# Kernel optimization log

Measured on AMD Instinct MI355X. Metric: run time of the kernel, lower is better.

The kernel has to match this reference:

```python
import jax, jax.numpy as jnp
import numpy as np

N = 50000      # nodes
E = 800000     # edges (avg degree 16)
D_IN = 64      # input feature dim
HID = 128      # hidden dim
NEG = 0.2      # LeakyReLU slope (PyG GATConv default)
EPS = 1e-5     # BatchNorm eps


def _bn(x, g, b):
    mu = jnp.mean(x, 0)
    var = jnp.var(x, 0)
    return (x - mu) * jax.lax.rsqrt(var + EPS) * g + b


def _gat(x, src, dst, W, a_s, a_d, bias, heads, out_c, concat):
    # PyG GATConv: h = xW per head, e_ij = LeakyReLU(a_s.h_i + a_d.h_j),
    # softmax over incoming edges of each dst node, weighted scatter-sum.
    n = x.shape[0]
    h = (x @ W).reshape(n, heads, out_c)                 # [N,H,C]
    sc_s = jnp.sum(h * a_s, -1)                          # [N,H]
    sc_d = jnp.sum(h * a_d, -1)                          # [N,H]
    e = jax.nn.leaky_relu(sc_s[src] + sc_d[dst], NEG)    # [E,H]
    m = jax.lax.stop_gradient(jax.ops.segment_max(e, dst, num_segments=n))
    e = jnp.exp(e - m[dst])
    s = jax.ops.segment_sum(e, dst, num_segments=n)
    alpha = e / (s[dst] + 1e-16)                         # [E,H]
    out = jax.ops.segment_sum(h[src] * alpha[:, :, None], dst, num_segments=n)
    out = out.reshape(n, heads * out_c) if concat else out.mean(1)
    return out + bias


def setup_inputs() -> dict:
    ks = jax.random.split(jax.random.key(0), 20)
    r = lambda i, sh, s=0.05: jax.random.normal(ks[i], sh, jnp.float32) * s
    return dict(
        x=jax.random.normal(ks[0], (N, D_IN), jnp.float32),
        edge_index=jax.random.randint(ks[1], (2, E), 0, N, dtype=jnp.int32),
        in_gamma=jnp.ones((D_IN,)), in_beta=jnp.zeros((D_IN,)),
        proj_W=r(2, (D_IN, HID)), proj_b=jnp.zeros((HID,)),
        skip_W=r(3, (HID, HID)), skip_b=jnp.zeros((HID,)),
        conv1_W=r(4, (HID, HID)), conv1_as=r(5, (4, 32)), conv1_ad=r(6, (4, 32)), conv1_b=jnp.zeros((HID,)),
        bn1_g=jnp.ones((HID,)), bn1_b=jnp.zeros((HID,)),
        conv2_W=r(7, (HID, HID)), conv2_as=r(8, (4, 32)), conv2_ad=r(9, (4, 32)), conv2_b=jnp.zeros((HID,)),
        bn2_g=jnp.ones((HID,)), bn2_b=jnp.zeros((HID,)),
        conv3_W=r(10, (HID, HID)), conv3_as=r(11, (1, HID)), conv3_ad=r(12, (1, HID)), conv3_b=jnp.zeros((HID,)),
        bn3_g=jnp.ones((HID,)), bn3_b=jnp.zeros((HID,)),
        cls_W1=r(13, (HID, 64)), cls_b1=jnp.zeros((64,)),
        cls_W2=r(14, (64, 32)), cls_b2=jnp.zeros((32,)),
        cls_W3=r(15, (32, 2)), cls_b3=jnp.zeros((2,)),
        conf_W=r(16, (HID, 1)), conf_b=jnp.zeros((1,)),
    )


def reference(x, edge_index, in_gamma, in_beta, proj_W, proj_b, skip_W, skip_b,
              conv1_W, conv1_as, conv1_ad, conv1_b, bn1_g, bn1_b,
              conv2_W, conv2_as, conv2_ad, conv2_b, bn2_g, bn2_b,
              conv3_W, conv3_as, conv3_ad, conv3_b, bn3_g, bn3_b,
              cls_W1, cls_b1, cls_W2, cls_b2, cls_W3, cls_b3, conf_W, conf_b):
    n = x.shape[0]
    # PyG GATConv add_self_loops=True
    loop = jnp.arange(n, dtype=edge_index.dtype)
    src = jnp.concatenate([edge_index[0], loop])
    dst = jnp.concatenate([edge_index[1], loop])

    h = _bn(x, in_gamma, in_beta)
    h = h @ proj_W + proj_b
    hr = jax.nn.relu(h)
    h_skip = hr @ skip_W + skip_b

    h = _gat(hr, src, dst, conv1_W, conv1_as, conv1_ad, conv1_b, 4, 32, True)
    h = jax.nn.relu(_bn(h, bn1_g, bn1_b))
    h = _gat(h, src, dst, conv2_W, conv2_as, conv2_ad, conv2_b, 4, 32, True)
    h = jax.nn.relu(_bn(h, bn2_g, bn2_b))
    h = _gat(h, src, dst, conv3_W, conv3_as, conv3_ad, conv3_b, 1, HID, False)
    h = jax.nn.relu(_bn(h, bn3_g, bn3_b) + h_skip)

    c = jax.nn.relu(h @ cls_W1 + cls_b1)
    c = jax.nn.relu(c @ cls_W2 + cls_b2)
    logits = c @ cls_W3 + cls_b3
    conf = jax.nn.sigmoid(h @ conf_W + conf_b)
    return logits, conf
```

## Files before the change

### kernel.cpp

```cpp
#include <hip/hip_runtime.h>
#include <cstdint>
#include <cstddef>

#define NN 50000
#define EE 800000
#define TOT_E (NN + EE)
#define NBK 391
#define BCAP 2560

typedef __attribute__((ext_vector_type(8))) short short8;
typedef __attribute__((ext_vector_type(4))) float f32x4;

static __device__ __forceinline__ unsigned short f2bf(float f) {
  union { float f; unsigned u; } v;
  v.f = f;
  unsigned r = v.u + 0x7FFFu + ((v.u >> 16) & 1u);
  return (unsigned short)(r >> 16);
}
static __device__ __forceinline__ float bf2f(unsigned short u) {
  union { unsigned u; float f; } v;
  v.u = ((unsigned)u) << 16;
  return v.f;
}
static __device__ __forceinline__ float bf2f_lo(unsigned u) {
  union { unsigned u; float f; } v;
  v.u = u << 16;
  return v.f;
}
static __device__ __forceinline__ float bf2f_hi(unsigned u) {
  union { unsigned u; float f; } v;
  v.u = u & 0xFFFF0000u;
  return v.f;
}

__global__ __launch_bounds__(512) void k_prep(
    const float* __restrict__ projW, const float* __restrict__ skipW,
    const float* __restrict__ c1W, const float* __restrict__ c2W,
    const float* __restrict__ c3W, const float* __restrict__ W1,
    const float* __restrict__ cw, unsigned short* __restrict__ wr,
    const float* __restrict__ x, float* __restrict__ xpart,
    const int* __restrict__ ei, int* __restrict__ gpos,
    unsigned* __restrict__ binned) {
  __shared__ float smf[1024];
  int tx = threadIdx.x;
  int b = blockIdx.x;
  if (b < 164) {
    int o = b * 512 + tx;
    if (o < 8192) {
      int off = o;
      int j = off & 7, t = off >> 3;
      int q = t & 3; t >>= 2;
      int c = t & 15; t >>= 4;
      int kb = t & 1, ct = t >> 1;
      int k = kb * 32 + q * 8 + j, col = ct * 16 + c;
      wr[o] = f2bf(projW[(size_t)k * 128 + col]);
    } else if (o < 73728) {
      int region = (o - 8192) >> 14;
      int off = (o - 8192) & 16383;
      const float* W = region == 0 ? skipW : region == 1 ? c1W : region == 2 ? c2W : c3W;
      int j = off & 7, t = off >> 3;
      int q = t & 3; t >>= 2;
      int c = t & 15; t >>= 4;
      int kb = t & 3, ct = t >> 2;
      int k = kb * 32 + q * 8 + j, col = ct * 16 + c;
      wr[o] = f2bf(W[(size_t)k * 128 + col]);
    } else if (o < 83968) {
      int off = o - 73728;
      int j = off & 7, t = off >> 3;
      int q = t & 3; t >>= 2;
      int c = t & 15; t >>= 4;
      int kb = t & 3, ct = t >> 2;
      int k = kb * 32 + q * 8 + j, col = ct * 16 + c;
      float v = 0.f;
      if (col < 64) v = W1[(size_t)k * 64 + col];
      else if (col == 64) v = cw[k];
      wr[o] = f2bf(v);
    }
  } else if (b < 292) {
    int bi = b - 164;
    int lane = tx & 63, wv = tx >> 6;
    int cg = lane & 15;
    int rsub = wv * 4 + (lane >> 4);
    int col4 = cg * 4;
    float s[4] = {0.f, 0.f, 0.f, 0.f}, q[4] = {0.f, 0.f, 0.f, 0.f};
    for (int r = bi * 32 + rsub; r < NN; r += 128 * 32) {
      float4 v = *(const float4*)(x + (size_t)r * 64 + col4);
      s[0] += v.x; q[0] += v.x * v.x;
      s[1] += v.y; q[1] += v.y * v.y;
      s[2] += v.z; q[2] += v.z * v.z;
      s[3] += v.w; q[3] += v.w * v.w;
    }
#pragma unroll
    for (int j = 0; j < 4; ++j) {
      s[j] += __shfl_xor(s[j], 16); s[j] += __shfl_xor(s[j], 32);
      q[j] += __shfl_xor(q[j], 16); q[j] += __shfl_xor(q[j], 32);
    }
    if (lane < 16) {
#pragma unroll
      for (int j = 0; j < 4; ++j) {
        smf[wv * 128 + col4 + j] = s[j];
        smf[wv * 128 + 64 + col4 + j] = q[j];
      }
    }
    __syncthreads();
    if (tx < 64) {
      float ss = 0.f, qq = 0.f;
#pragma unroll
      for (int w = 0; w < 8; ++w) {
        ss += smf[w * 128 + tx];
        qq += smf[w * 128 + 64 + tx];
      }
      xpart[bi * 128 + tx] = ss;
      xpart[bi * 128 + 64 + tx] = qq;
    }
  } else {
    int* cnt = (int*)smf;
    int* base = (int*)smf + 512;
    cnt[tx] = 0;
    __syncthreads();
    int e0 = (b - 292) * 3125;
    int e1 = e0 + 3125;
    if (e1 > EE) e1 = EE;
    for (int i = e0 + tx; i < e1; i += 512) {
      int d = ei[EE + i];
      atomicAdd(&cnt[d >> 7], 1);
    }
    __syncthreads();
    if (tx < NBK) {
      int c = cnt[tx];
      base[tx] = c ? atomicAdd(&gpos[tx], c) : 0;
      cnt[tx] = 0;
    }
    __syncthreads();
    for (int i = e0 + tx; i < e1; i += 512) {
      int s = ei[i];
      int d = ei[EE + i];
      int bk = d >> 7;
      int slot = base[bk] + atomicAdd(&cnt[bk], 1);
      if (slot < BCAP)
        binned[(size_t)bk * BCAP + slot] = (unsigned)s | ((unsigned)(d & 127) << 16);
    }
  }
}

__global__ __launch_bounds__(256) void k_bucket(const unsigned* __restrict__ binned,
                                                const int* __restrict__ gpos,
                                                int* __restrict__ rowp,
                                                int* __restrict__ srcl) {
  __shared__ int cnt[128], offs[128], cur[128];
  __shared__ int red[256], red2[256];
  int b = blockIdx.x, tid = threadIdx.x;
  int accp = 0, acct = 0;
  for (int i = tid; i < NBK; i += 256) {
    int gv = gpos[i];
    if (gv > BCAP) gv = BCAP;
    if (i < b) accp += gv;
    acct += gv;
  }
  red[tid] = accp;
  red2[tid] = acct;
  __syncthreads();
  for (int o = 128; o; o >>= 1) {
    if (tid < o) {
      red[tid] += red[tid + o];
      red2[tid] += red2[tid + o];
    }
    __syncthreads();
  }
  int eb = (b << 7) + red[0];
  if (b == NBK - 1 && tid == 0) rowp[NN] = red2[0] + NN;

  int n0 = b << 7;
  int nodes = NN - n0;
  if (nodes > 128) nodes = 128;
  int ne = gpos[b];
  if (ne > BCAP) ne = BCAP;
  if (tid < 128) cnt[tid] = (tid < nodes) ? 1 : 0;
  __syncthreads();
  const unsigned* bb = binned + (size_t)b * BCAP;
  for (int i = tid; i < ne; i += 256) atomicAdd(&cnt[bb[i] >> 16], 1);
  __syncthreads();
  if (tid < 128) offs[tid] = cnt[tid];
  __syncthreads();
  for (int o = 1; o < 128; o <<= 1) {
    int t = (tid < 128 && tid >= o) ? offs[tid - o] : 0;
    __syncthreads();
    if (tid < 128) offs[tid] += t;
    __syncthreads();
  }
  if (tid < 128 && tid < nodes) {
    int ex = offs[tid] - cnt[tid];
    rowp[n0 + tid] = eb + ex;
    srcl[eb + ex] = n0 + tid;
    cur[tid] = ex + 1;
  }
  __syncthreads();
  for (int i = tid; i < ne; i += 256) {
    unsigned e = bb[i];
    int r = atomicAdd(&cur[e >> 16], 1);
    srcl[eb + r] = (int)(e & 0xFFFFu);
  }
}

template <int NH, int NT, int F>
static __device__ __forceinline__ void write_scores(const f32x4 (&acc)[F][NT],
                                                    const float* __restrict__ a_s,
                                                    const float* __restrict__ a_d,
                                                    int r0, int lane, int wv,
                                                    float* __restrict__ scs,
                                                    float* __restrict__ scd) {
  const int lr = lane & 15, lg = lane >> 4;
  float asv[NT], adv[NT];
#pragma unroll
  for (int ct = 0; ct < NT; ++ct) {
    asv[ct] = a_s[ct * 16 + lr];
    adv[ct] = a_d[ct * 16 + lr];
  }
  float ps[F][4][NH], pd[F][4][NH];
#pragma unroll
  for (int f = 0; f < F; ++f)
#pragma unroll
    for (int r = 0; r < 4; ++r)
#pragma unroll
      for (int h = 0; h < NH; ++h) { ps[f][r][h] = 0.f; pd[f][r][h] = 0.f; }
#pragma unroll
  for (int f = 0; f < F; ++f)
#pragma unroll
    for (int ct = 0; ct < NT; ++ct) {
      int h = (NH == 1) ? 0 : (ct >> 1);
#pragma unroll
      for (int r = 0; r < 4; ++r) {
        ps[f][r][h] = fmaf(acc[f][ct][r], asv[ct], ps[f][r][h]);
        pd[f][r][h] = fmaf(acc[f][ct][r], adv[ct], pd[f][r][h]);
      }
    }
#pragma unroll
  for (int off = 1; off < 16; off <<= 1)
#pragma unroll
    for (int f = 0; f < F; ++f)
#pragma unroll
      for (int r = 0; r < 4; ++r)
#pragma unroll
        for (int h = 0; h < NH; ++h) {
          ps[f][r][h] += __shfl_xor(ps[f][r][h], off);
          pd[f][r][h] += __shfl_xor(pd[f][r][h], off);
        }
  if (lr == 0) {
#pragma unroll
    for (int f = 0; f < F; ++f) {
      int rowb = r0 + (wv * F + f) * 16 + lg * 4;
#pragma unroll
      for (int r = 0; r < 4; ++r) {
        int gr = rowb + r;
        if (gr < NN) {
          if (NH == 4) {
            float4 vs = make_float4(ps[f][r][0], ps[f][r][1], ps[f][r][2], ps[f][r][3]);
            float4 vd = make_float4(pd[f][r][0], pd[f][r][1], pd[f][r][2], pd[f][r][3]);
            *(float4*)(scs + (size_t)gr * 4) = vs;
            *(float4*)(scd + (size_t)gr * 4) = vd;
          } else {
            scs[gr] = ps[f][r][0];
            scd[gr] = pd[f][r][0];
          }
        }
      }
    }
  }
}

template <int BIAS, int RELU, int NT, int F>
static __device__ __forceinline__ void write_out_bf(const f32x4 (&acc)[F][NT],
                                                    const float* __restrict__ bias,
                                                    int r0, int lane, int wv,
                                                    unsigned short* __restrict__ out) {
  const int lr = lane & 15, lg = lane >> 4;
#pragma unroll
  for (int f = 0; f < F; ++f) {
    int rowb = r0 + (wv * F + f) * 16 + lg * 4;
#pragma unroll
    for (int ct = 0; ct < NT; ++ct) {
      int col = ct * 16 + lr;
      float bb = BIAS ? bias[col] : 0.f;
#pragma unroll
      for (int r = 0; r < 4; ++r) {
        int gr = rowb + r;
        if (gr < NN) {
          float o = acc[f][ct][r] + bb;
          if (RELU) o = fmaxf(o, 0.f);
          out[(size_t)gr * 128 + col] = f2bf(o);
        }
      }
    }
  }
}

__global__ __launch_bounds__(256) void k_front(
    const float* __restrict__ x, const float* __restrict__ xpart,
    const float* __restrict__ in_g, const float* __restrict__ in_b,
    const unsigned short* __restrict__ BwP, const float* __restrict__ projb,
    const unsigned short* __restrict__ BwS, const float* __restrict__ skipb,
    const unsigned short* __restrict__ BwC, const float* __restrict__ a_s,
    const float* __restrict__ a_d,
    unsigned short* __restrict__ hsk, unsigned short* __restrict__ hb,
    float* __restrict__ scs, float* __restrict__ scd) {
  __shared__ __align__(16) unsigned short sm[32768];
  __shared__ float bnsc[64], bnsh[64];
  const int tid = threadIdx.x;
  const int r0 = blockIdx.x * 128;

  if (tid < 64) {
    float s = 0.f, q = 0.f;
#pragma unroll 8
    for (int pp = 0; pp < 128; ++pp) {
      s += xpart[pp * 128 + tid];
      q += xpart[pp * 128 + 64 + tid];
    }
    float invM = 1.f / (float)NN;
    float mu = s * invM;
    float var = q * invM - mu * mu;
    float sc = in_g[tid] * rsqrtf(var + 1e-5f);
    bnsc[tid] = sc;
    bnsh[tid] = in_b[tid] - mu * sc;
  }
  __syncthreads();

#pragma unroll
  for (int it = 0; it < 8; ++it) {
    int idx = it * 256 + tid;
    int r = idx >> 4;
    int k = (idx & 15) * 4;
    int gr = r0 + r;
    float4 av = make_float4(0.f, 0.f, 0.f, 0.f);
    if (gr < NN) av = *(const float4*)(x + (size_t)gr * 64 + k);
    av.x = av.x * bnsc[k + 0] + bnsh[k + 0];
    av.y = av.y * bnsc[k + 1] + bnsh[k + 1];
    av.z = av.z * bnsc[k + 2] + bnsh[k + 2];
    av.w = av.w * bnsc[k + 3] + bnsh[k + 3];
    ushort4 o;
    o.x = f2bf(av.x); o.y = f2bf(av.y); o.z = f2bf(av.z); o.w = f2bf(av.w);
    *(ushort4*)&sm[((r >> 4) * 2 + (k >> 5)) * 512 + (r & 15) * 32 + (k & 31)] = o;
  }
#pragma unroll
  for (int it = 0; it < 4; ++it) {
    int idx = it * 256 + tid;
    *(uint4*)&sm[8192 + idx * 8] = *(const uint4*)(BwP + idx * 8);
  }
  __syncthreads();

  const int lane = tid & 63, wv = tid >> 6;
  const int lr = lane & 15, lg = lane >> 4;
  const int fidx = lr * 32 + lg * 8;
  f32x4 acc[2][8];
#pragma unroll
  for (int f = 0; f < 2; ++f)
#pragma unroll
    for (int ct = 0; ct < 8; ++ct) acc[f][ct] = (f32x4){0.f, 0.f, 0.f, 0.f};
#pragma unroll
  for (int kb = 0; kb < 2; ++kb) {
    short8 a0 = *(const short8*)&sm[((wv * 2 + 0) * 2 + kb) * 512 + fidx];
    short8 a1 = *(const short8*)&sm[((wv * 2 + 1) * 2 + kb) * 512 + fidx];
#pragma unroll
    for (int ct = 0; ct < 8; ++ct) {
      short8 b = *(const short8*)&sm[8192 + (ct * 2 + kb) * 512 + fidx];
      acc[0][ct] = __builtin_amdgcn_mfma_f32_16x16x32_bf16(a0, b, acc[0][ct], 0, 0, 0);
      acc[1][ct] = __builtin_amdgcn_mfma_f32_16x16x32_bf16(a1, b, acc[1][ct], 0, 0, 0);
    }
  }
  __syncthreads();

  {
    float pbv[8];
#pragma unroll
    for (int ct = 0; ct < 8; ++ct) pbv[ct] = projb[ct * 16 + lr];
#pragma unroll
    for (int f = 0; f < 2; ++f) {
      int rowb = (wv * 2 + f) * 16 + lg * 4;
#pragma unroll
      for (int ct = 0; ct < 8; ++ct) {
        int col = ct * 16 + lr;
#pragma unroll
        for (int r = 0; r < 4; ++r) {
          int row = rowb + r;
          float o = fmaxf(acc[f][ct][r] + pbv[ct], 0.f);
          sm[((row >> 4) * 4 + (col >> 5)) * 512 + (row & 15) * 32 + (col & 31)] = f2bf(o);
        }
      }
    }
  }
#pragma unroll
  for (int it = 0; it < 8; ++it) {
    int idx = it * 256 + tid;
    *(uint4*)&sm[16384 + idx * 8] = *(const uint4*)(BwS + idx * 8);
  }
  __syncthreads();

#pragma unroll
  for (int f = 0; f < 2; ++f)
#pragma unroll
    for (int ct = 0; ct < 8; ++ct) acc[f][ct] = (f32x4){0.f, 0.f, 0.f, 0.f};
#pragma unroll
  for (int kb = 0; kb < 4; ++kb) {
    short8 a0 = *(const short8*)&sm[((wv * 2 + 0) * 4 + kb) * 512 + fidx];
    short8 a1 = *(const short8*)&sm[((wv * 2 + 1) * 4 + kb) * 512 + fidx];
#pragma unroll
    for (int ct = 0; ct < 8; ++ct) {
      short8 b = *(const short8*)&sm[16384 + (ct * 4 + kb) * 512 + fidx];
      acc[0][ct] = __builtin_amdgcn_mfma_f32_16x16x32_bf16(a0, b, acc[0][ct], 0, 0, 0);
      acc[1][ct] = __builtin_amdgcn_mfma_f32_16x16x32_bf16(a1, b, acc[1][ct], 0, 0, 0);
    }
  }
  write_out_bf<1, 0>(acc, skipb, r0, lane, wv, hsk);
  __syncthreads();

#pragma unroll
  for (int it = 0; it < 8; ++it) {
    int idx = it * 256 + tid;
    *(uint4*)&sm[16384 + idx * 8] = *(const uint4*)(BwC + idx * 8);
  }
  __syncthreads();

#pragma unroll
  for (int f = 0; f < 2; ++f)
#pragma unroll
    for (int ct = 0; ct < 8; ++ct) acc[f][ct] = (f32x4){0.f, 0.f, 0.f, 0.f};
#pragma unroll
  for (int kb = 0; kb < 4; ++kb) {
    short8 a0 = *(const short8*)&sm[((wv * 2 + 0) * 4 + kb) * 512 + fidx];
    short8 a1 = *(const short8*)&sm[((wv * 2 + 1) * 4 + kb) * 512 + fidx];
#pragma unroll
    for (int ct = 0; ct < 8; ++ct) {
      short8 b = *(const short8*)&sm[16384 + (ct * 4 + kb) * 512 + fidx];
      acc[0][ct] = __builtin_amdgcn_mfma_f32_16x16x32_bf16(a0, b, acc[0][ct], 0, 0, 0);
      acc[1][ct] = __builtin_amdgcn_mfma_f32_16x16x32_bf16(a1, b, acc[1][ct], 0, 0, 0);
    }
  }
  write_scores<4>(acc, a_s, a_d, r0, lane, wv, scs, scd);
  write_out_bf<0, 0>(acc, nullptr, r0, lane, wv, hb);
}

template <int BM, int K, int NT, int ABF, int BN, int BNP, int BIAS, int RELU, int OUTM, int SCH>
__global__ __launch_bounds__(256) void k_mgemm(
    const void* __restrict__ Ain, const unsigned short* __restrict__ Bw,
    const float* __restrict__ bias,
    const float* __restrict__ bnsums, const float* __restrict__ bng,
    const float* __restrict__ bnb,
    const unsigned short* __restrict__ skip,
    const float* __restrict__ a_s, const float* __restrict__ a_d,
    const float* __restrict__ confb,
    void* __restrict__ Cout, float* __restrict__ conf,
    float* __restrict__ scs, float* __restrict__ scd,
    const float* __restrict__ W2, const float* __restrict__ b2,
    const float* __restrict__ W3, const float* __restrict__ b3,
    float* __restrict__ logits) {
  constexpr int KB = K / 32;
  constexpr int RT = BM / 16;
  constexpr int F = BM / 64;
  __shared__ __align__(16) unsigned short sm[(RT + NT) * KB * 512];
  __shared__ float bnsc[128], bnsh[128];
  const int tid = threadIdx.x;
  const int r0 = blockIdx.x * BM;

  if constexpr (BN) {
    if (tid < K) {
      float s = 0.f, q = 0.f;
#pragma unroll 8
      for (int pp = 0; pp < 32; ++pp) {
        s += bnsums[pp * 256 + tid];
        q += bnsums[pp * 256 + 128 + tid];
      }
      float invM = 1.f / (float)NN;
      float mu = s * invM;
      float var = q * invM - mu * mu;
      float sc = bng[tid] * rsqrtf(var + 1e-5f);
      bnsc[tid] = sc;
      bnsh[tid] = bnb[tid] - mu * sc;
    }
    __syncthreads();
  }

  {
    const unsigned short* A = (const unsigned short*)Ain;
    constexpr int IT = BM * (K / 8) / 256;
#pragma unroll
    for (int it = 0; it < IT; ++it) {
      int idx = it * 256 + tid;
      int r = idx / (K / 8);
      int k = (idx % (K / 8)) * 8;
      int gr = r0 + r;
      union { uint4 u4; unsigned short us[8]; } v;
      v.u4 = make_uint4(0, 0, 0, 0);
      if (gr < NN) v.u4 = *(const uint4*)(A + (size_t)gr * K + k);
      if constexpr (BN) {
        union { uint4 u4; unsigned short us[8]; } sv;
        if (BN == 3) {
          sv.u4 = make_uint4(0, 0, 0, 0);
          if (gr < NN) sv.u4 = *(const uint4*)(skip + (size_t)gr * 128 + k);
        }
#pragma unroll
        for (int j = 0; j < 8; ++j) {
          float f = bf2f(v.us[j]) * bnsc[k + j] + bnsh[k + j];
          if (BN == 3) f += bf2f(sv.us[j]);
          if (BN >= 2) f = fmaxf(f, 0.f);
          v.us[j] = f2bf(f);
        }
      }
      *(uint4*)&sm[((r >> 4) * KB + (k >> 5)) * 512 + (r & 15) * 32 + (k & 31)] = v.u4;
    }
  }
  {
    constexpr int BW = NT * KB * 512;
#pragma unroll
    for (int it = 0; it < BW / 2048; ++it) {
      int idx = it * 256 + tid;
      *(uint4*)&sm[RT * KB * 512 + idx * 8] = *(const uint4*)(Bw + idx * 8);
    }
  }
  __syncthreads();

  const int lane = tid & 63, wv = tid >> 6;
  const int lr = lane & 15, lg = lane >> 4;
  const int fidx = lr * 32 + lg * 8;
  f32x4 acc[F][NT];
#pragma unroll
  for (int f = 0; f < F; ++f)
#pragma unroll
    for (int ct = 0; ct < NT; ++ct) acc[f][ct] = (f32x4){0.f, 0.f, 0.f, 0.f};
#pragma unroll
  for (int kb = 0; kb < KB; ++kb) {
    short8 afr[F];
#pragma unroll
    for (int f = 0; f < F; ++f)
      afr[f] = *(const short8*)&sm[((wv * F + f) * KB + kb) * 512 + fidx];
#pragma unroll
    for (int ct = 0; ct < NT; ++ct) {
      short8 b = *(const short8*)&sm[((RT + ct) * KB + kb) * 512 + fidx];
#pragma unroll
      for (int f = 0; f < F; ++f)
        acc[f][ct] = __builtin_amdgcn_mfma_f32_16x16x32_bf16(afr[f], b, acc[f][ct], 0, 0, 0);
    }
  }

  if constexpr (SCH > 0) {
    write_scores<(SCH == 1) ? 1 : 4>(acc, a_s, a_d, r0, lane, wv, scs, scd);
  }

  if constexpr (OUTM == 2) {
    __syncthreads();
    unsigned short* c1s = sm;
    float* W2s = (float*)(sm + 8320);
    float* c2s = (float*)(sm + 12416);
    float* W3s = (float*)(sm + 20864);
    float* b2s = (float*)(sm + 20992);
    float* b3s = (float*)(sm + 21056);
    for (int i = tid; i < 2048; i += 256) W2s[i] = W2[i];
    if (tid < 64) W3s[tid] = W3[tid];
    if (tid < 32) b2s[tid] = b2[tid];
    if (tid < 2) b3s[tid] = b3[tid];
#pragma unroll
    for (int f = 0; f < F; ++f) {
      int lrow = (wv * F + f) * 16 + lg * 4;
#pragma unroll
      for (int ct = 0; ct < NT; ++ct) {
        int col = ct * 16 + lr;
        if (col < 64) {
          float bb = bias[col];
#pragma unroll
          for (int r = 0; r < 4; ++r)
            c1s[(lrow + r) * 65 + col] = f2bf(fmaxf(acc[f][ct][r] + bb, 0.f));
        } else if (col == 64) {
          float cb = confb[0];
#pragma unroll
          for (int r = 0; r < 4; ++r) {
            int gr = r0 + lrow + r;
            if (gr < NN) conf[gr] = 1.f / (1.f + __expf(-(acc[f][ct][r] + cb)));
          }
        }
      }
    }
    __syncthreads();
    {
      int node = tid & 127;
      int cb = (tid >> 7) * 16;
      float a2[16];
#pragma unroll
      for (int i = 0; i < 16; ++i) a2[i] = b2s[cb + i];
      for (int k = 0; k < 64; ++k) {
        float v = bf2f(c1s[node * 65 + k]);
#pragma unroll
        for (int i = 0; i < 16; ++i) a2[i] = fmaf(v, W2s[k * 32 + cb + i], a2[i]);
      }
#pragma unroll
      for (int i = 0; i < 16; ++i) c2s[node * 33 + cb + i] = fmaxf(a2[i], 0.f);
    }
    __syncthreads();
    {
      int node = tid >> 1, j = tid & 1;
      float s3 = b3s[j];
#pragma unroll 8
      for (int k = 0; k < 32; ++k) s3 = fmaf(c2s[node * 33 + k], W3s[k * 2 + j], s3);
      int gr = r0 + node;
      if (gr < NN) logits[(size_t)gr * 2 + j] = s3;
    }
  } else {
    write_out_bf<BIAS, RELU>(acc, bias, r0, lane, wv, (unsigned short*)Cout);
  }
}

template <int H>
__global__ __launch_bounds__(256) void k_agg(const unsigned short* __restrict__ hp,
                                             const float* __restrict__ scs,
                                             const float* __restrict__ scd,
                                             const int* __restrict__ rowp,
                                             const int* __restrict__ srcl,
                                             const float* __restrict__ bias,
                                             unsigned short* __restrict__ out,
                                             float* __restrict__ part) {
  __shared__ float ssum[8][144], ssq[8][144];
  int tid = threadIdx.x;
  int lane = tid & 63, wv = tid >> 6;
  int half = lane >> 5;
  int l32 = lane & 31;
  int g = l32 >> 4;
  int l16 = lane & 15;
  int n = (blockIdx.x * 4 + wv) * 2 + half;
  int c0 = l16 * 8;
  int hid = (H == 1) ? 0 : (l16 >> 2);
  float sd = scd[(size_t)n * H + hid];
  int beg = rowp[n], end = rowp[n + 1];
  int last = end - 1;
  float a[8];
#pragma unroll
  for (int i = 0; i < 8; ++i) a[i] = 0.f;
  float sw = 0.f;
  int k0 = beg + g * 4;
  int s0 = srcl[(k0 + 0) <= last ? (k0 + 0) : last];
  int s1 = srcl[(k0 + 1) <= last ? (k0 + 1) : last];
  int s2 = srcl[(k0 + 2) <= last ? (k0 + 2) : last];
  int s3 = srcl[(k0 + 3) <= last ? (k0 + 3) : last];
  for (; k0 < end; k0 += 8) {
    int np = k0 + 8;
    int t0 = srcl[(np + 0) <= last ? (np + 0) : last];
    int t1 = srcl[(np + 1) <= last ? (np + 1) : last];
    int t2 = srcl[(np + 2) <= last ? (np + 2) : last];
    int t3 = srcl[(np + 3) <= last ? (np + 3) : last];
    float e0 = scs[(size_t)s0 * H + hid] + sd;
    float e1 = scs[(size_t)s1 * H + hid] + sd;
    float e2 = scs[(size_t)s2 * H + hid] + sd;
    float e3 = scs[(size_t)s3 * H + hid] + sd;
    uint4 u0 = *(const uint4*)(hp + (size_t)s0 * 128 + c0);
    uint4 u1 = *(const uint4*)(hp + (size_t)s1 * 128 + c0);
    uint4 u2 = *(const uint4*)(hp + (size_t)s2 * 128 + c0);
    uint4 u3 = *(const uint4*)(hp + (size_t)s3 * 128 + c0);
    e0 = fmaxf(e0, 0.f) + 0.2f * fminf(e0, 0.f);
    e1 = fmaxf(e1, 0.f) + 0.2f * fminf(e1, 0.f);
    e2 = fmaxf(e2, 0.f) + 0.2f * fminf(e2, 0.f);
    e3 = fmaxf(e3, 0.f) + 0.2f * fminf(e3, 0.f);
    float w0 = __expf(e0);
    float w1 = (k0 + 1 <= last) ? __expf(e1) : 0.f;
    float w2 = (k0 + 2 <= last) ? __expf(e2) : 0.f;
    float w3 = (k0 + 3 <= last) ? __expf(e3) : 0.f;
    a[0] = fmaf(w0, bf2f_lo(u0.x), a[0]); a[1] = fmaf(w0, bf2f_hi(u0.x), a[1]);
    a[2] = fmaf(w0, bf2f_lo(u0.y), a[2]); a[3] = fmaf(w0, bf2f_hi(u0.y), a[3]);
    a[4] = fmaf(w0, bf2f_lo(u0.z), a[4]); a[5] = fmaf(w0, bf2f_hi(u0.z), a[5]);
    a[6] = fmaf(w0, bf2f_lo(u0.w), a[6]); a[7] = fmaf(w0, bf2f_hi(u0.w), a[7]);
    a[0] = fmaf(w1, bf2f_lo(u1.x), a[0]); a[1] = fmaf(w1, bf2f_hi(u1.x), a[1]);
    a[2] = fmaf(w1, bf2f_lo(u1.y), a[2]); a[3] = fmaf(w1, bf2f_hi(u1.y), a[3]);
    a[4] = fmaf(w1, bf2f_lo(u1.z), a[4]); a[5] = fmaf(w1, bf2f_hi(u1.z), a[5]);
    a[6] = fmaf(w1, bf2f_lo(u1.w), a[6]); a[7] = fmaf(w1, bf2f_hi(u1.w), a[7]);
    a[0] = fmaf(w2, bf2f_lo(u2.x), a[0]); a[1] = fmaf(w2, bf2f_hi(u2.x), a[1]);
    a[2] = fmaf(w2, bf2f_lo(u2.y), a[2]); a[3] = fmaf(w2, bf2f_hi(u2.y), a[3]);
    a[4] = fmaf(w2, bf2f_lo(u2.z), a[4]); a[5] = fmaf(w2, bf2f_hi(u2.z), a[5]);
    a[6] = fmaf(w2, bf2f_lo(u2.w), a[6]); a[7] = fmaf(w2, bf2f_hi(u2.w), a[7]);
    a[0] = fmaf(w3, bf2f_lo(u3.x), a[0]); a[1] = fmaf(w3, bf2f_hi(u3.x), a[1]);
    a[2] = fmaf(w3, bf2f_lo(u3.y), a[2]); a[3] = fmaf(w3, bf2f_hi(u3.y), a[3]);
    a[4] = fmaf(w3, bf2f_lo(u3.z), a[4]); a[5] = fmaf(w3, bf2f_hi(u3.z), a[5]);
    a[6] = fmaf(w3, bf2f_lo(u3.w), a[6]); a[7] = fmaf(w3, bf2f_hi(u3.w), a[7]);
    sw += (w0 + w1) + (w2 + w3);
    s0 = t0; s1 = t1; s2 = t2; s3 = t3;
  }
#pragma unroll
  for (int i = 0; i < 8; ++i) a[i] += __shfl_xor(a[i], 16);
  sw += __shfl_xor(sw, 16);
  int slice = wv * 2 + half;
  if (g == 0) {
    float inv = 1.f / (sw + 1e-16f);
    unsigned wb[4];
    int ib = c0 + l16;
#pragma unroll
    for (int j = 0; j < 4; ++j) {
      float o0 = a[2 * j] * inv + bias[c0 + 2 * j];
      float o1 = a[2 * j + 1] * inv + bias[c0 + 2 * j + 1];
      ssum[slice][ib + 2 * j] = o0;
      ssum[slice][ib + 2 * j + 1] = o1;
      ssq[slice][ib + 2 * j] = o0 * o0;
      ssq[slice][ib + 2 * j + 1] = o1 * o1;
      wb[j] = (unsigned)f2bf(o0) | ((unsigned)f2bf(o1) << 16);
    }
    *(uint4*)(out + (size_t)n * 128 + c0) = make_uint4(wb[0], wb[1], wb[2], wb[3]);
  }
  __syncthreads();
  if (tid < 128) {
    int idx = tid + (tid >> 3);
    float s = 0.f, q = 0.f;
#pragma unroll
    for (int sl = 0; sl < 8; ++sl) {
      s += ssum[sl][idx];
      q += ssq[sl][idx];
    }
    int pb = (blockIdx.x & 31) * 256;
    atomicAdd(&part[pb + tid], s);
    atomicAdd(&part[pb + 128 + tid], q);
  }
}

extern "C" void kernel_launch(void* const* d_in, const int* in_sizes, int n_in,
                              void* d_out, int out_size, void* d_ws, size_t ws_size,
                              hipStream_t stream) {
  (void)in_sizes; (void)n_in; (void)out_size; (void)ws_size;
  const float* x       = (const float*)d_in[0];
  const int*   ei      = (const int*)d_in[1];
  const float* in_g    = (const float*)d_in[2];
  const float* in_b    = (const float*)d_in[3];
  const float* projW   = (const float*)d_in[4];
  const float* projb   = (const float*)d_in[5];
  const float* skipW   = (const float*)d_in[6];
  const float* skipb   = (const float*)d_in[7];
  const float* c1W     = (const float*)d_in[8];
  const float* c1as    = (const float*)d_in[9];
  const float* c1ad    = (const float*)d_in[10];
  const float* c1b     = (const float*)d_in[11];
  const float* bn1g    = (const float*)d_in[12];
  const float* bn1b    = (const float*)d_in[13];
  const float* c2W     = (const float*)d_in[14];
  const float* c2as    = (const float*)d_in[15];
  const float* c2ad    = (const float*)d_in[16];
  const float* c2b     = (const float*)d_in[17];
  const float* bn2g    = (const float*)d_in[18];
  const float* bn2b    = (const float*)d_in[19];
  const float* c3W     = (const float*)d_in[20];
  const float* c3as    = (const float*)d_in[21];
  const float* c3ad    = (const float*)d_in[22];
  const float* c3b     = (const float*)d_in[23];
  const float* bn3g    = (const float*)d_in[24];
  const float* bn3b    = (const float*)d_in[25];
  const float* clsW1   = (const float*)d_in[26];
  const float* clsb1   = (const float*)d_in[27];
  const float* clsW2   = (const float*)d_in[28];
  const float* clsb2   = (const float*)d_in[29];
  const float* clsW3   = (const float*)d_in[30];
  const float* clsb3   = (const float*)d_in[31];
  const float* confW   = (const float*)d_in[32];
  const float* confb   = (const float*)d_in[33];

  float* out_logits = (float*)d_out;
  float* out_conf   = (float*)d_out + (size_t)NN * 2;

  char* p = (char*)d_ws;
  auto alloc = [&](size_t bytes) -> char* {
    char* r = p;
    p += (bytes + 255) & ~(size_t)255;
    return r;
  };
  unsigned short* hsk = (unsigned short*)alloc((size_t)NN * 128 * 2);
  unsigned short* hb  = (unsigned short*)alloc((size_t)NN * 128 * 2);
  unsigned short* agA = (unsigned short*)alloc((size_t)NN * 128 * 2);
  unsigned short* agB = (unsigned short*)alloc((size_t)NN * 128 * 2);
  float* scs   = (float*)alloc((size_t)NN * 4 * 4);
  float* scd   = (float*)alloc((size_t)NN * 4 * 4);
  char*  zr    = alloc(2048 + 3 * 32768);
  int*   gpos  = (int*)zr;
  float* part1 = (float*)(zr + 2048);
  float* part2 = part1 + 8192;
  float* part3 = part2 + 8192;
  float* xpart = (float*)alloc(128 * 128 * 4);
  int*   rowp  = (int*)alloc((size_t)(NN + 1) * 4);
  unsigned* binned = (unsigned*)alloc((size_t)NBK * BCAP * 4);
  int*   srcl  = (int*)alloc((size_t)TOT_E * 4);
  unsigned short* wr = (unsigned short*)alloc(83968 * 2);
  unsigned short* wr_proj = wr;
  unsigned short* wr_skip = wr + 8192;
  unsigned short* wr_c1   = wr + 24576;
  unsigned short* wr_c2   = wr + 40960;
  unsigned short* wr_c3   = wr + 57344;
  unsigned short* wr_cls  = wr + 73728;

  const int GB64  = (NN + 63) / 64;
  const int GB128 = (NN + 127) / 128;
  const int AB    = NN / 8;

  hipMemsetAsync(zr, 0, 2048 + 3 * 32768, stream);

  k_prep<<<548, 512, 0, stream>>>(projW, skipW, c1W, c2W, c3W, clsW1, confW, wr,
                                  x, xpart, ei, gpos, binned);
  k_bucket<<<NBK, 256, 0, stream>>>(binned, gpos, rowp, srcl);

  k_front<<<GB128, 256, 0, stream>>>(x, xpart, in_g, in_b, wr_proj, projb,
                                     wr_skip, skipb, wr_c1, c1as, c1ad,
                                     hsk, hb, scs, scd);
  k_agg<4><<<AB, 256, 0, stream>>>(hb, scs, scd, rowp, srcl, c1b, agA, part1);

  k_mgemm<64, 128, 8, 1, 2, 1, 0, 0, 1, 4><<<GB64, 256, 0, stream>>>(
      agA, wr_c2, nullptr, part1, bn1g, bn1b, nullptr, c2as, c2ad, nullptr,
      hb, nullptr, scs, scd, nullptr, nullptr, nullptr, nullptr, nullptr);
  k_agg<4><<<AB, 256, 0, stream>>>(hb, scs, scd, rowp, srcl, c2b, agB, part2);

  k_mgemm<64, 128, 8, 1, 2, 1, 0, 0, 1, 1><<<GB64, 256, 0, stream>>>(
      agB, wr_c3, nullptr, part2, bn2g, bn2b, nullptr, c3as, c3ad, nullptr,
      hb, nullptr, scs, scd, nullptr, nullptr, nullptr, nullptr, nullptr);
  k_agg<1><<<AB, 256, 0, stream>>>(hb, scs, scd, rowp, srcl, c3b, agA, part3);

  k_mgemm<128, 128, 5, 1, 3, 1, 1, 0, 2, 0><<<GB128, 256, 0, stream>>>(
      agA, wr_cls, clsb1, part3, bn3g, bn3b, hsk, nullptr, nullptr, confb,
      nullptr, out_conf, nullptr, nullptr, clsW2, clsb2, clsW3, clsb3, out_logits);
}
```

Before: 223.2 us.

## Merge CSR bucketing into front kernel and fold partial zeroing into prep

Removes the separate k_bucket launch by running the CSR bucketing as extra blocks of k_front, which overlap with the front GEMM blocks. The input BatchNorm statistics are now accumulated with atomics into a small xsum buffer, replacing the per-block partial array that k_front had to reduce. The zeroing of the later partial buffers moves from the memset into dedicated k_prep blocks, so the memset only clears a small region. The edge binning in k_prep is split over twice as many blocks. Float atomics make the statistics order nondeterministic, and the extra blocks add some imbalance.

New measurement: 216.4 us. 1.03x faster.

```diff
diff --git a/kernel.cpp b/kernel.cpp
--- a/kernel.cpp
+++ b/kernel.cpp
@@ -38,7 +38,8 @@
     const float* __restrict__ c1W, const float* __restrict__ c2W,
     const float* __restrict__ c3W, const float* __restrict__ W1,
     const float* __restrict__ cw, unsigned short* __restrict__ wr,
-    const float* __restrict__ x, float* __restrict__ xpart,
+    const float* __restrict__ x, float* __restrict__ xsum,
+    float* __restrict__ partz,
     const int* __restrict__ ei, int* __restrict__ gpos,
     unsigned* __restrict__ binned) {
   __shared__ float smf[1024];
@@ -110,16 +111,18 @@
         ss += smf[w * 128 + tx];
         qq += smf[w * 128 + 64 + tx];
       }
-      xpart[bi * 128 + tx] = ss;
-      xpart[bi * 128 + 64 + tx] = qq;
-    }
+      atomicAdd(&xsum[tx], ss);
+      atomicAdd(&xsum[64 + tx], qq);
+    }
+  } else if (b < 340) {
+    partz[(b - 292) * 512 + tx] = 0.f;
   } else {
     int* cnt = (int*)smf;
     int* base = (int*)smf + 512;
     cnt[tx] = 0;
     __syncthreads();
-    int e0 = (b - 292) * 3125;
-    int e1 = e0 + 3125;
+    int e0 = (b - 340) * 1563;
+    int e1 = e0 + 1563;
     if (e1 > EE) e1 = EE;
     for (int i = e0 + tx; i < e1; i += 512) {
       int d = ei[EE + i];
@@ -140,65 +143,6 @@
       if (slot < BCAP)
         binned[(size_t)bk * BCAP + slot] = (unsigned)s | ((unsigned)(d & 127) << 16);
     }
-  }
-}
-
-__global__ __launch_bounds__(256) void k_bucket(const unsigned* __restrict__ binned,
-                                                const int* __restrict__ gpos,
-                                                int* __restrict__ rowp,
-                                                int* __restrict__ srcl) {
-  __shared__ int cnt[128], offs[128], cur[128];
-  __shared__ int red[256], red2[256];
-  int b = blockIdx.x, tid = threadIdx.x;
-  int accp = 0, acct = 0;
-  for (int i = tid; i < NBK; i += 256) {
-    int gv = gpos[i];
-    if (gv > BCAP) gv = BCAP;
-    if (i < b) accp += gv;
-    acct += gv;
-  }
-  red[tid] = accp;
-  red2[tid] = acct;
-  __syncthreads();
-  for (int o = 128; o; o >>= 1) {
-    if (tid < o) {
-      red[tid] += red[tid + o];
-      red2[tid] += red2[tid + o];
-    }
-    __syncthreads();
-  }
-  int eb = (b << 7) + red[0];
-  if (b == NBK - 1 && tid == 0) rowp[NN] = red2[0] + NN;
-
-  int n0 = b << 7;
-  int nodes = NN - n0;
-  if (nodes > 128) nodes = 128;
-  int ne = gpos[b];
-  if (ne > BCAP) ne = BCAP;
-  if (tid < 128) cnt[tid] = (tid < nodes) ? 1 : 0;
-  __syncthreads();
-  const unsigned* bb = binned + (size_t)b * BCAP;
-  for (int i = tid; i < ne; i += 256) atomicAdd(&cnt[bb[i] >> 16], 1);
-  __syncthreads();
-  if (tid < 128) offs[tid] = cnt[tid];
-  __syncthreads();
-  for (int o = 1; o < 128; o <<= 1) {
-    int t = (tid < 128 && tid >= o) ? offs[tid - o] : 0;
-    __syncthreads();
-    if (tid < 128) offs[tid] += t;
-    __syncthreads();
-  }
-  if (tid < 128 && tid < nodes) {
-    int ex = offs[tid] - cnt[tid];
-    rowp[n0 + tid] = eb + ex;
-    srcl[eb + ex] = n0 + tid;
-    cur[tid] = ex + 1;
-  }
-  __syncthreads();
-  for (int i = tid; i < ne; i += 256) {
-    unsigned e = bb[i];
-    int r = atomicAdd(&cur[e >> 16], 1);
-    srcl[eb + r] = (int)(e & 0xFFFFu);
   }
 }
 
@@ -295,29 +239,85 @@
 }
 
 __global__ __launch_bounds__(256) void k_front(
-    const float* __restrict__ x, const float* __restrict__ xpart,
+    const float* __restrict__ x, const float* __restrict__ xsum,
     const float* __restrict__ in_g, const float* __restrict__ in_b,
     const unsigned short* __restrict__ BwP, const float* __restrict__ projb,
     const unsigned short* __restrict__ BwS, const float* __restrict__ skipb,
     const unsigned short* __restrict__ BwC, const float* __restrict__ a_s,
     const float* __restrict__ a_d,
     unsigned short* __restrict__ hsk, unsigned short* __restrict__ hb,
-    float* __restrict__ scs, float* __restrict__ scd) {
+    float* __restrict__ scs, float* __restrict__ scd,
+    const unsigned* __restrict__ binned, const int* __restrict__ gpos,
+    int* __restrict__ rowp, int* __restrict__ srcl) {
   __shared__ __align__(16) unsigned short sm[32768];
   __shared__ float bnsc[64], bnsh[64];
   const int tid = threadIdx.x;
+
+  if (blockIdx.x >= 391) {
+    int* cnt  = (int*)sm;
+    int* offs = (int*)sm + 128;
+    int* cur  = (int*)sm + 256;
+    int* red  = (int*)sm + 384;
+    int* red2 = (int*)sm + 640;
+    int b = blockIdx.x - 391;
+    int accp = 0, acct = 0;
+    for (int i = tid; i < NBK; i += 256) {
+      int gv = gpos[i];
+      if (gv > BCAP) gv = BCAP;
+      if (i < b) accp += gv;
+      acct += gv;
+    }
+    red[tid] = accp;
+    red2[tid] = acct;
+    __syncthreads();
+    for (int o = 128; o; o >>= 1) {
+      if (tid < o) {
+        red[tid] += red[tid + o];
+        red2[tid] += red2[tid + o];
+      }
+      __syncthreads();
+    }
+    int eb = (b << 7) + red[0];
+    if (b == NBK - 1 && tid == 0) rowp[NN] = red2[0] + NN;
+
+    int n0 = b << 7;
+    int nodes = NN - n0;
+    if (nodes > 128) nodes = 128;
+    int ne = gpos[b];
+    if (ne > BCAP) ne = BCAP;
+    if (tid < 128) cnt[tid] = (tid < nodes) ? 1 : 0;
+    __syncthreads();
+    const unsigned* bb = binned + (size_t)b * BCAP;
+    for (int i = tid; i < ne; i += 256) atomicAdd(&cnt[bb[i] >> 16], 1);
+    __syncthreads();
+    if (tid < 128) offs[tid] = cnt[tid];
+    __syncthreads();
+    for (int o = 1; o < 128; o <<= 1) {
+      int t = (tid < 128 && tid >= o) ? offs[tid - o] : 0;
+      __syncthreads();
+      if (tid < 128) offs[tid] += t;
+      __syncthreads();
+    }
+    if (tid < 128 && tid < nodes) {
+      int ex = offs[tid] - cnt[tid];
+      rowp[n0 + tid] = eb + ex;
+      srcl[eb + ex] = n0 + tid;
+      cur[tid] = ex + 1;
+    }
+    __syncthreads();
+    for (int i = tid; i < ne; i += 256) {
+      unsigned e = bb[i];
+      int r = atomicAdd(&cur[e >> 16], 1);
+      srcl[eb + r] = (int)(e & 0xFFFFu);
+    }
+    return;
+  }
+
   const int r0 = blockIdx.x * 128;
-
   if (tid < 64) {
-    float s = 0.f, q = 0.f;
-#pragma unroll 8
-    for (int pp = 0; pp < 128; ++pp) {
-      s += xpart[pp * 128 + tid];
-      q += xpart[pp * 128 + 64 + tid];
-    }
     float invM = 1.f / (float)NN;
-    float mu = s * invM;
-    float var = q * invM - mu * mu;
+    float mu = xsum[tid] * invM;
+    float var = xsum[64 + tid] * invM - mu * mu;
     float sc = in_g[tid] * rsqrtf(var + 1e-5f);
     bnsc[tid] = sc;
     bnsh[tid] = in_b[tid] - mu * sc;
@@ -767,12 +767,12 @@
   unsigned short* agB = (unsigned short*)alloc((size_t)NN * 128 * 2);
   float* scs   = (float*)alloc((size_t)NN * 4 * 4);
   float* scd   = (float*)alloc((size_t)NN * 4 * 4);
-  char*  zr    = alloc(2048 + 3 * 32768);
+  char*  zr    = alloc(2048 + 512);
   int*   gpos  = (int*)zr;
-  float* part1 = (float*)(zr + 2048);
+  float* xsum  = (float*)(zr + 2048);
+  float* part1 = (float*)alloc(3 * 32768);
   float* part2 = part1 + 8192;
   float* part3 = part2 + 8192;
-  float* xpart = (float*)alloc(128 * 128 * 4);
   int*   rowp  = (int*)alloc((size_t)(NN + 1) * 4);
   unsigned* binned = (unsigned*)alloc((size_t)NBK * BCAP * 4);
   int*   srcl  = (int*)alloc((size_t)TOT_E * 4);
@@ -788,15 +788,15 @@
   const int GB128 = (NN + 127) / 128;
   const int AB    = NN / 8;
 
-  hipMemsetAsync(zr, 0, 2048 + 3 * 32768, stream);
-
-  k_prep<<<548, 512, 0, stream>>>(projW, skipW, c1W, c2W, c3W, clsW1, confW, wr,
-                                  x, xpart, ei, gpos, binned);
-  k_bucket<<<NBK, 256, 0, stream>>>(binned, gpos, rowp, srcl);
-
-  k_front<<<GB128, 256, 0, stream>>>(x, xpart, in_g, in_b, wr_proj, projb,
-                                     wr_skip, skipb, wr_c1, c1as, c1ad,
-                                     hsk, hb, scs, scd);
+  hipMemsetAsync(zr, 0, 2048 + 512, stream);
+
+  k_prep<<<852, 512, 0, stream>>>(projW, skipW, c1W, c2W, c3W, clsW1, confW, wr,
+                                  x, xsum, part1, ei, gpos, binned);
+
+  k_front<<<782, 256, 0, stream>>>(x, xsum, in_g, in_b, wr_proj, projb,
+                                   wr_skip, skipb, wr_c1, c1as, c1ad,
+                                   hsk, hb, scs, scd,
+                                   binned, gpos, rowp, srcl);
   k_agg<4><<<AB, 256, 0, stream>>>(hb, scs, scd, rowp, srcl, c1b, agA, part1);
 
   k_mgemm<64, 128, 8, 1, 2, 1, 0, 0, 1, 4><<<GB64, 256, 0, stream>>>(
```
